# Performance work log

Hardware: AMD Instinct MI355X
Metric: run time of the kernel (lower is better)

Reference implementation:

```python
import jax, jax.numpy as jnp
import numpy as np

ITERS = 10


def setup_inputs() -> dict:
    key = jax.random.key(0)
    k0, k1 = jax.random.split(key)
    B, D, H, W = 4, 64, 64, 64
    feat0 = jax.random.normal(k0, (B, D, H, W), dtype=jnp.float32)
    feat1 = jax.random.normal(k1, (B, D, H, W), dtype=jnp.float32)
    bin_score = jnp.asarray(1.0, dtype=jnp.float32)  # learned scalar parameter
    return {"feat0": feat0, "feat1": feat1, "bin_score": bin_score}


def _cdist(x, y):
    # torch.cdist(p=2): euclidean distance between rows. x: [b,m,d], y: [b,n,d]
    x2 = jnp.sum(x * x, axis=-1)[:, :, None]          # [b,m,1]
    y2 = jnp.sum(y * y, axis=-1)[:, None, :]          # [b,1,n]
    xy = jnp.einsum('bmd,bnd->bmn', x, y)             # [b,m,n]
    d2 = jnp.maximum(x2 + y2 - 2.0 * xy, 0.0)
    return jnp.sqrt(d2)


def _log_sinkhorn(Z, log_mu, log_nu, iters):
    # Z: [b, m+1, n+1]; log_mu: [b, m+1]; log_nu: [b, n+1]
    u0 = jnp.zeros_like(log_mu)
    v0 = jnp.zeros_like(log_nu)

    def body(i, uv):
        u, v = uv
        u = log_mu - jax.nn.logsumexp(Z + v[:, None, :], axis=2)
        v = log_nu - jax.nn.logsumexp(Z + u[:, :, None], axis=1)
        return (u, v)

    u, v = jax.lax.fori_loop(0, iters, body, (u0, v0))
    return Z + u[:, :, None] + v[:, None, :]


def _forward(feat0, feat1, bin_score):
    b, d, h, w = feat0.shape
    f0 = feat0.transpose(0, 2, 3, 1).reshape(b, h * w, d)
    f1 = feat1.transpose(0, 2, 3, 1).reshape(b, h * w, d)
    distance = _cdist(f0, f1)                         # [b, m, n]
    m, n = h * w, h * w
    dt = distance.dtype

    bins0 = jnp.broadcast_to(bin_score, (b, m, 1)).astype(dt)
    bins1 = jnp.broadcast_to(bin_score, (b, 1, n)).astype(dt)
    binsa = jnp.broadcast_to(bin_score, (b, 1, 1)).astype(dt)
    couplings = jnp.concatenate([
        jnp.concatenate([distance, bins0], axis=-1),
        jnp.concatenate([bins1, binsa], axis=-1),
    ], axis=1)                                        # [b, m+1, n+1]

    ms = jnp.asarray(m, dt)
    ns = jnp.asarray(n, dt)
    norm = -jnp.log(ms + ns)
    log_mu = jnp.concatenate([jnp.full((m,), norm, dtype=dt), (jnp.log(ns) + norm)[None]])
    log_nu = jnp.concatenate([jnp.full((n,), norm, dtype=dt), (jnp.log(ms) + norm)[None]])
    log_mu = jnp.broadcast_to(log_mu[None], (b, m + 1))
    log_nu = jnp.broadcast_to(log_nu[None], (b, n + 1))

    Z = _log_sinkhorn(couplings, log_mu, log_nu, ITERS)
    Z = Z - norm
    gamma = jnp.exp(Z)                                # [b, m+1, n+1]

    matching_loss = jnp.mean(jnp.sum(gamma[:, :-1, :-1] * distance, axis=2))
    dustbin_loss = jnp.mean(gamma[:, :, -1]) + jnp.mean(gamma[:, :-1, :])
    return matching_loss, dustbin_loss, gamma


def reference(feat0, feat1, bin_score):
    return _forward(feat0, feat1, bin_score)
```

## Files before the change

kernel.cpp:

```cpp
#include <hip/hip_runtime.h>
#include <math.h>

#define BB 4
#define DD 64
#define MM 4096
#define M1 4097
#define NORMC 9.0109133472792788f
#define CSH 11.0f
#define SCLX 1.0e12f
#define INVSCLX 1.0e-12f

typedef __attribute__((ext_vector_type(8))) short bf16x8;
typedef __attribute__((ext_vector_type(4))) float f32x4;

__device__ __forceinline__ f32x4 mfma16(bf16x8 a, bf16x8 b, f32x4 c) {
    return __builtin_amdgcn_mfma_f32_16x16x32_bf16(a, b, c, 0, 0, 0);
}
__device__ __forceinline__ unsigned short f2bf(float x) {
    unsigned u = __float_as_uint(x);
    u += 0x7fffu + ((u >> 16) & 1u);
    return (unsigned short)(u >> 16);
}

__global__ void __launch_bounds__(256)
prep_kernel(const float* __restrict__ f0, const float* __restrict__ f1,
            unsigned short* __restrict__ h0, unsigned short* __restrict__ h1) {
    __shared__ float T[64][65];
    const int b = blockIdx.y;
    const int p0 = blockIdx.x * 64;
    const float* src = (blockIdx.z == 0 ? f0 : f1) + (size_t)b * DD * MM;
    unsigned short* dh = (blockIdx.z == 0 ? h0 : h1) + (size_t)b * MM * DD;
    const int tid = threadIdx.x;
#pragma unroll
    for (int l = 0; l < 16; ++l) {
        int idx = l * 256 + tid;
        T[idx >> 6][idx & 63] = src[(idx >> 6) * MM + p0 + (idx & 63)];
    }
    __syncthreads();
    const int p = tid >> 2;
    const int cs = (tid & 3) * 16;
    unsigned hw[8];
#pragma unroll
    for (int k = 0; k < 8; ++k) {
        unsigned short a = f2bf(T[cs + 2 * k][p]);
        unsigned short c = f2bf(T[cs + 2 * k + 1][p]);
        hw[k] = (unsigned)a | ((unsigned)c << 16);
    }
    size_t base = (size_t)(p0 + p) * DD + cs;
    *(uint4*)(dh + base)     = make_uint4(hw[0], hw[1], hw[2], hw[3]);
    *(uint4*)(dh + base + 8) = make_uint4(hw[4], hw[5], hw[6], hw[7]);
}

__global__ void __launch_bounds__(256)
norms_kernel(const float* __restrict__ f0, const float* __restrict__ f1,
             float* __restrict__ n0, float* __restrict__ n1,
             float* __restrict__ W, float* __restrict__ S) {
    int t = blockIdx.x * 256 + threadIdx.x;
    if (t >= BB * MM) return;
    int b = t / MM, p = t % MM;
    const float* s0 = f0 + (size_t)b * DD * MM + p;
    const float* s1 = f1 + (size_t)b * DD * MM + p;
    float a = 0.f, c = 0.f;
#pragma unroll 8
    for (int k = 0; k < DD; ++k) {
        float x = s0[(size_t)k * MM]; a = fmaf(x, x, a);
        float y = s1[(size_t)k * MM]; c = fmaf(y, y, c);
    }
    n0[t] = a; n1[t] = c;
    W[t] = 1.0f;
    if (t < 8) S[t] = 1.0f;
}

__global__ void __launch_bounds__(256)
distEB_kernel(const unsigned short* __restrict__ h0, const unsigned short* __restrict__ h1,
              const float* __restrict__ n0, const float* __restrict__ n1,
              uint2* __restrict__ EB) {
    __shared__ unsigned char sc[4][640];
    const int id = blockIdx.x;
    const int xcd = id & 7, slot = id >> 3;
    const int b = xcd >> 1;
    const int x = slot * 2 + (xcd & 1);
    const int r0 = x * 32;
    const int tid = threadIdx.x;
    const int w = tid >> 6, l = tid & 63, lg = l >> 4, lc = l & 15;
    const size_t fb = (size_t)b * MM * DD;

    bf16x8 Ah[2][2];
    float n0r[2][4];
#pragma unroll
    for (int st = 0; st < 2; ++st) {
        const unsigned short* pa = h0 + fb + (size_t)(r0 + st * 16 + lc) * DD + 8 * lg;
        Ah[st][0] = *(const bf16x8*)pa; Ah[st][1] = *(const bf16x8*)(pa + 32);
#pragma unroll
        for (int e = 0; e < 4; ++e)
            n0r[st][e] = n0[b * MM + r0 + st * 16 + 4 * lg + e];
    }

    for (int tt = 0; tt < 64; ++tt) {
        const int jt = w * 64 + tt;
        const int j0 = jt * 16;
        const unsigned short* pb = h1 + fb + (size_t)(j0 + lc) * DD + 8 * lg;
        bf16x8 Bh0 = *(const bf16x8*)pb, Bh1 = *(const bf16x8*)(pb + 32);
        float n1j = n1[b * MM + j0 + lc];
        unsigned pk[2];
#pragma unroll
        for (int st = 0; st < 2; ++st) {
            f32x4 acc = {0.f, 0.f, 0.f, 0.f};
            acc = mfma16(Ah[st][0], Bh0, acc);
            acc = mfma16(Ah[st][1], Bh1, acc);
            float Ev[4];
#pragma unroll
            for (int e = 0; e < 4; ++e) {
                float d2 = fmaxf(__builtin_fmaf(-2.f, acc[e], n0r[st][e] + n1j), 0.f);
                Ev[e] = __expf(sqrtf(d2) - CSH);
            }
            int p = __builtin_amdgcn_cvt_pk_fp8_f32(Ev[0], Ev[1], 0, false);
            p = __builtin_amdgcn_cvt_pk_fp8_f32(Ev[2], Ev[3], p, true);
            pk[st] = (unsigned)p;
        }
        *(unsigned*)&sc[w][lc * 40 + 4 * lg]      = pk[0];
        *(unsigned*)&sc[w][lc * 40 + 16 + 4 * lg] = pk[1];
        uint2 v = *(const uint2*)&sc[w][lc * 40 + 8 * lg];
        EB[(((size_t)(b * 128 + x)) * 256 + jt) * 64 + l] = v;
    }
}

__global__ void __launch_bounds__(512)
sinkEB_kernel(const uint2* __restrict__ EB, const float* __restrict__ W,
              float* __restrict__ X, float* __restrict__ S,
              float* __restrict__ psum, const float* __restrict__ bin) {
    const int bid = blockIdx.x;
    const int tid = threadIdx.x;
    const float bs = *bin;
    if (bid < BB) {
        __shared__ float am[8];
        const int b = bid;
        const int w = tid >> 6, l = tid & 63;
        float s = 0.f;
        for (int t = tid; t < MM; t += 512) s += W[b * MM + t];
#pragma unroll
        for (int off = 1; off < 64; off <<= 1) s += __shfl_xor(s, off);
        if (l == 0) am[w] = s;
        __syncthreads();
        if (tid == 0) {
            float tot = 0.f;
#pragma unroll
            for (int k = 0; k < 8; ++k) tot += am[k];
            S[b] = 0.5f * __expf(-bs) / (tot + S[4 + b]);
        }
        return;
    }
    __shared__ float Wl[4096];
    __shared__ float ps[256];
    __shared__ float XL[32];
    const int idx = bid - BB;
    const int b = idx >> 7, x = idx & 127;
    const int w = tid >> 6, l = tid & 63, lg = l >> 4, lc = l & 15;
    const float KC = __expf(-NORMC - CSH);
    const float wmm = __expf(bs - CSH) * S[4 + b];
#pragma unroll
    for (int k = 0; k < 8; ++k) Wl[k * 512 + tid] = W[b * MM + k * 512 + tid];
    __syncthreads();

    const uint2* EP = EB + (((size_t)(b * 128 + x)) * 256 + w * 32) * 64 + l;
    uint2 ec[32];
#pragma unroll
    for (int k = 0; k < 32; ++k) ec[k] = EP[(size_t)k * 64];

    float rs[8] = {};
#pragma unroll
    for (int k = 0; k < 32; ++k) {
        float wv = Wl[(w * 32 + k) * 16 + lc];
        auto p0 = __builtin_amdgcn_cvt_pk_f32_fp8((int)ec[k].x, false);
        auto p1 = __builtin_amdgcn_cvt_pk_f32_fp8((int)ec[k].x, true);
        auto p2 = __builtin_amdgcn_cvt_pk_f32_fp8((int)ec[k].y, false);
        auto p3 = __builtin_amdgcn_cvt_pk_f32_fp8((int)ec[k].y, true);
        rs[0] = fmaf(p0[0], wv, rs[0]); rs[1] = fmaf(p0[1], wv, rs[1]);
        rs[2] = fmaf(p1[0], wv, rs[2]); rs[3] = fmaf(p1[1], wv, rs[3]);
        rs[4] = fmaf(p2[0], wv, rs[4]); rs[5] = fmaf(p2[1], wv, rs[5]);
        rs[6] = fmaf(p3[0], wv, rs[6]); rs[7] = fmaf(p3[1], wv, rs[7]);
    }
#pragma unroll
    for (int off = 1; off < 16; off <<= 1)
#pragma unroll
        for (int t = 0; t < 8; ++t) rs[t] += __shfl_xor(rs[t], off);
    if (lc == 0) {
#pragma unroll
        for (int t = 0; t < 8; ++t) ps[w * 32 + 8 * lg + t] = rs[t];
    }
    __syncthreads();
    if (tid < 32) {
        float s = 0.f;
#pragma unroll
        for (int k = 0; k < 8; ++k) s += ps[k * 32 + tid];
        float xv = KC / (s + wmm);
        X[b * MM + x * 32 + tid] = xv;
        XL[tid] = xv * SCLX;
    }
    __syncthreads();

    float f0 = XL[8 * lg + 0], f1 = XL[8 * lg + 1];
    float f2 = XL[8 * lg + 2], f3 = XL[8 * lg + 3];
    float f4 = XL[8 * lg + 4], f5 = XL[8 * lg + 5];
    float f6 = XL[8 * lg + 6], f7 = XL[8 * lg + 7];
    int u0 = __builtin_amdgcn_cvt_pk_fp8_f32(f0, f1, 0, false);
    u0 = __builtin_amdgcn_cvt_pk_fp8_f32(f2, f3, u0, true);
    int u1 = __builtin_amdgcn_cvt_pk_fp8_f32(f4, f5, 0, false);
    u1 = __builtin_amdgcn_cvt_pk_fp8_f32(f6, f7, u1, true);
    long long av = (long long)(((unsigned long long)(unsigned)u1 << 32) | (unsigned)u0);
    float* po = psum + ((size_t)(b * 128 + x)) * MM;
    const f32x4 zero = {0.f, 0.f, 0.f, 0.f};
#pragma unroll
    for (int k = 0; k < 32; ++k) {
        long long bv = (long long)(((unsigned long long)ec[k].y << 32) | ec[k].x);
        f32x4 c = __builtin_amdgcn_mfma_f32_16x16x32_fp8_fp8(av, bv, zero, 0, 0, 0);
        if (l < 16) po[(w * 32 + k) * 16 + l] = c[0];
    }
}

__global__ void __launch_bounds__(256)
wcomb_kernel(const float* __restrict__ psum, const float* __restrict__ X,
             float* __restrict__ W, float* __restrict__ S,
             const float* __restrict__ bin) {
    const int bid = blockIdx.x;
    const int tid = threadIdx.x;
    const float bs = *bin;
    if (bid < BB * 64) {
        __shared__ float ps[256];
        const int b = bid >> 6, cg = bid & 63;
        const int c64 = tid & 63, g = tid >> 6;
        const float* pp = psum + ((size_t)(b * 128 + g * 32)) * MM + cg * 64 + c64;
        float s = 0.f;
#pragma unroll
        for (int c = 0; c < 32; ++c) s += pp[(size_t)c * MM];
        ps[tid] = s;
        __syncthreads();
        if (tid < 64) {
            float t = ps[tid] + ps[tid + 64] + ps[tid + 128] + ps[tid + 192];
            t = t * INVSCLX + __expf(bs - CSH) * S[b];
            W[b * MM + cg * 64 + tid] = __expf(-NORMC - CSH) / t;
        }
    } else {
        const int b = bid - BB * 64;
        const int w = tid >> 6, l = tid & 63;
        __shared__ float am[4];
        float s = 0.f;
        for (int t = tid; t < MM; t += 256) s += X[b * MM + t];
#pragma unroll
        for (int off = 1; off < 64; off <<= 1) s += __shfl_xor(s, off);
        if (l == 0) am[w] = s;
        __syncthreads();
        if (tid == 0) {
            float tot = am[0] + am[1] + am[2] + am[3];
            S[4 + b] = 0.5f * __expf(-bs) / (tot + S[b]);
        }
    }
}

__global__ void __launch_bounds__(256)
finEB_kernel(const uint2* __restrict__ EB, const float* __restrict__ X,
             const float* __restrict__ W, const float* __restrict__ S,
             const float* __restrict__ bin, float* __restrict__ G,
             float* __restrict__ pA, float* __restrict__ pB) {
    const int bid = blockIdx.x;
    const int tid = threadIdx.x;
    if (bid >= BB * 128) {
        const int eb = bid - BB * 128;
        const float bs = *bin;
        const float CC = __expf(NORMC + bs);
        int t = eb * 256 + tid;
        float pc = 0.f, pr = 0.f;
        if (t < BB * M1) {
            int b = t / M1, j = t % M1;
            float wj = (j < MM) ? W[b * MM + j] : S[4 + b];
            float g = CC * S[b] * wj;
            G[((size_t)b * M1 + MM) * M1 + j] = g;
            if (j == MM) pc += g;
        } else if (t < BB * M1 + BB * MM) {
            int q = t - BB * M1;
            int b = q / MM, i = q % MM;
            float g = CC * X[b * MM + i] * S[4 + b];
            G[((size_t)b * M1 + i) * M1 + MM] = g;
            pc += g; pr += g;
        }
#pragma unroll
        for (int off = 1; off < 64; off <<= 1) {
            pc += __shfl_xor(pc, off);
            pr += __shfl_xor(pr, off);
        }
        __shared__ float e0[4], e1[4];
        if ((tid & 63) == 0) { e0[tid >> 6] = pc; e1[tid >> 6] = pr; }
        __syncthreads();
        if (tid == 0) {
            pB[eb * 2 + 0] = e0[0] + e0[1] + e0[2] + e0[3];
            pB[eb * 2 + 1] = e1[0] + e1[1] + e1[2] + e1[3];
        }
        return;
    }
    __shared__ float T[256][36];
    __shared__ float Wl[4096];
    __shared__ float XL[32];
    const int b = bid >> 7, x = bid & 127;
    const int w = tid >> 6, l = tid & 63, lg = l >> 4, lc = l & 15;
#pragma unroll
    for (int k = 0; k < 16; ++k) Wl[k * 256 + tid] = W[b * MM + k * 256 + tid];
    if (tid < 32) XL[tid] = X[b * MM + x * 32 + tid] * __expf(NORMC + CSH);
    __syncthreads();

    const uint2* EBb = EB + ((size_t)(b * 128 + x)) * 256 * 64;
    float pm = 0.f, pr = 0.f;
    for (int ch = 0; ch < 16; ++ch) {
#pragma unroll
        for (int q = 0; q < 4; ++q) {
            const int jt = ch * 16 + w * 4 + q;
            uint2 ev = EBb[(size_t)jt * 64 + l];
            float wv = Wl[jt * 16 + lc];
            auto p0 = __builtin_amdgcn_cvt_pk_f32_fp8((int)ev.x, false);
            auto p1 = __builtin_amdgcn_cvt_pk_f32_fp8((int)ev.x, true);
            auto p2 = __builtin_amdgcn_cvt_pk_f32_fp8((int)ev.y, false);
            auto p3 = __builtin_amdgcn_cvt_pk_f32_fp8((int)ev.y, true);
            float Ef[8] = {p0[0], p0[1], p1[0], p1[1], p2[0], p2[1], p3[0], p3[1]};
            float g[8];
#pragma unroll
            for (int t = 0; t < 8; ++t) {
                g[t] = Ef[t] * XL[8 * lg + t] * wv;
                pm = fmaf(g[t], (Ef[t] > 0.f) ? (CSH + __logf(Ef[t])) : 0.f, pm);
                pr += g[t];
            }
            const int jl = (w * 4 + q) * 16 + lc;
            f32x4 v0 = {g[0], g[1], g[2], g[3]};
            f32x4 v1 = {g[4], g[5], g[6], g[7]};
            *(f32x4*)&T[jl][8 * lg]     = v0;
            *(f32x4*)&T[jl][8 * lg + 4] = v1;
        }
        __syncthreads();
        float* gb = G + ((size_t)(b * M1 + x * 32)) * M1 + ch * 256 + tid;
#pragma unroll
        for (int r = 0; r < 32; ++r) gb[(size_t)r * M1] = T[tid][r];
        __syncthreads();
    }
#pragma unroll
    for (int off = 1; off < 64; off <<= 1) {
        pm += __shfl_xor(pm, off);
        pr += __shfl_xor(pr, off);
    }
    __shared__ float s0[4], s1[4];
    if (l == 0) { s0[w] = pm; s1[w] = pr; }
    __syncthreads();
    if (tid == 0) {
        pA[bid * 2 + 0] = s0[0] + s0[1] + s0[2] + s0[3];
        pA[bid * 2 + 1] = s1[0] + s1[1] + s1[2] + s1[3];
    }
}

__global__ void __launch_bounds__(256)
reduce_out_kernel(const float* __restrict__ pA, int nA,
                  const float* __restrict__ pB, int nB, float* __restrict__ out) {
    const int tid = threadIdx.x;
    float pm = 0.f, prA = 0.f, pc = 0.f, prB = 0.f;
    for (int r = tid; r < nA; r += 256) { pm += pA[2 * r]; prA += pA[2 * r + 1]; }
    for (int r = tid; r < nB; r += 256) { pc += pB[2 * r]; prB += pB[2 * r + 1]; }
#pragma unroll
    for (int off = 1; off < 64; off <<= 1) {
        pm += __shfl_xor(pm, off);
        prA += __shfl_xor(prA, off);
        pc += __shfl_xor(pc, off);
        prB += __shfl_xor(prB, off);
    }
    __shared__ float a0[4], a1[4], a2[4], a3[4];
    if ((tid & 63) == 0) {
        int w = tid >> 6;
        a0[w] = pm; a1[w] = prA; a2[w] = pc; a3[w] = prB;
    }
    __syncthreads();
    if (tid == 0) {
        float PM = a0[0] + a0[1] + a0[2] + a0[3];
        float PRA = a1[0] + a1[1] + a1[2] + a1[3];
        float PC = a2[0] + a2[1] + a2[2] + a2[3];
        float PRB = a3[0] + a3[1] + a3[2] + a3[3];
        out[0] = PM / (4.0f * 4096.0f);
        out[1] = PC / (4.0f * 4097.0f) + (PRA + PRB) / (4.0f * 4096.0f * 4097.0f);
    }
}

extern "C" void kernel_launch(void* const* d_in, const int* in_sizes, int n_in,
                              void* d_out, int out_size, void* d_ws, size_t ws_size,
                              hipStream_t stream) {
    const float* feat0 = (const float*)d_in[0];
    const float* feat1 = (const float*)d_in[1];
    const float* bin   = (const float*)d_in[2];
    float* out = (float*)d_out;
    float* G   = out + 2;
    float* ws  = (float*)d_ws;

    const size_t OF_X   = 0;
    const size_t OF_W   = 16384;
    const size_t OF_S   = 32768;
    const size_t OF_PA  = 32832;
    const size_t OF_PB  = 33856;
    const size_t OF_N0  = 34128;
    const size_t OF_N1  = 50512;
    const size_t OF_PS  = 66896;
    const size_t OF_BF  = 2164048;
    const size_t OF_E8  = 3212624;

    float* X    = ws + OF_X;
    float* W    = ws + OF_W;
    float* S    = ws + OF_S;
    float* pA   = ws + OF_PA;
    float* pB   = ws + OF_PB;
    float* n0   = ws + OF_N0;
    float* n1   = ws + OF_N1;
    float* psum = ws + OF_PS;
    unsigned short* h0 = (unsigned short*)(ws + OF_BF);
    unsigned short* h1 = h0 + 1048576;
    uint2* EB = (uint2*)(ws + OF_E8);

    prep_kernel<<<dim3(64, BB, 2), 256, 0, stream>>>(feat0, feat1, h0, h1);
    norms_kernel<<<64, 256, 0, stream>>>(feat0, feat1, n0, n1, W, S);
    distEB_kernel<<<512, 256, 0, stream>>>(h0, h1, n0, n1, EB);
    for (int it = 0; it < 10; ++it) {
        sinkEB_kernel<<<BB + BB * 128, 512, 0, stream>>>(EB, W, X, S, psum, bin);
        wcomb_kernel<<<BB * 64 + BB, 256, 0, stream>>>(psum, X, W, S, bin);
    }
    finEB_kernel<<<BB * 128 + 129, 256, 0, stream>>>(EB, X, W, S, bin, G, pA, pB);
    reduce_out_kernel<<<1, 256, 0, stream>>>(pA, BB * 128, pB, 129, out);
}
```

Baseline: 384.0 us.

## Fuse Sinkhorn column combine into row kernel via atomic column sums

Removes the separate wcomb kernel per iteration by having each row block atomically add its column partial sums into a per-iteration buffer. The next iteration's kernel recomputes W and the dustbin scalars from those sums, which halves the launches per iteration and drops the large psum round trip through memory. The cost is that every block recomputes the full W vector and its reduction, and the atomics make the floating-point summation order nondeterministic. A memset now zeroes the per-iteration sum buffers.

```diff
diff --git a/kernel.cpp b/kernel.cpp
--- a/kernel.cpp
+++ b/kernel.cpp
@@ -53,8 +53,7 @@
 
 __global__ void __launch_bounds__(256)
 norms_kernel(const float* __restrict__ f0, const float* __restrict__ f1,
-             float* __restrict__ n0, float* __restrict__ n1,
-             float* __restrict__ W, float* __restrict__ S) {
+             float* __restrict__ n0, float* __restrict__ n1) {
     int t = blockIdx.x * 256 + threadIdx.x;
     if (t >= BB * MM) return;
     int b = t / MM, p = t % MM;
@@ -67,8 +66,6 @@
         float y = s1[(size_t)k * MM]; c = fmaf(y, y, c);
     }
     n0[t] = a; n1[t] = c;
-    W[t] = 1.0f;
-    if (t < 8) S[t] = 1.0f;
 }
 
 __global__ void __launch_bounds__(256)
@@ -126,41 +123,59 @@
 }
 
 __global__ void __launch_bounds__(512)
-sinkEB_kernel(const uint2* __restrict__ EB, const float* __restrict__ W,
-              float* __restrict__ X, float* __restrict__ S,
-              float* __restrict__ psum, const float* __restrict__ bin) {
-    const int bid = blockIdx.x;
-    const int tid = threadIdx.x;
-    const float bs = *bin;
-    if (bid < BB) {
-        __shared__ float am[8];
-        const int b = bid;
-        const int w = tid >> 6, l = tid & 63;
-        float s = 0.f;
-        for (int t = tid; t < MM; t += 512) s += W[b * MM + t];
-#pragma unroll
-        for (int off = 1; off < 64; off <<= 1) s += __shfl_xor(s, off);
-        if (l == 0) am[w] = s;
-        __syncthreads();
-        if (tid == 0) {
-            float tot = 0.f;
-#pragma unroll
-            for (int k = 0; k < 8; ++k) tot += am[k];
-            S[b] = 0.5f * __expf(-bs) / (tot + S[4 + b]);
-        }
-        return;
-    }
+sinkF_kernel(const uint2* __restrict__ EB,
+             const float* __restrict__ csPrev, float* __restrict__ csCur,
+             const float* __restrict__ sxpPrev, float* __restrict__ sxpCur,
+             const float* __restrict__ xmmPrev, float* __restrict__ xmmCur,
+             float* __restrict__ X, const float* __restrict__ bin, int first) {
     __shared__ float Wl[4096];
     __shared__ float ps[256];
     __shared__ float XL[32];
-    const int idx = bid - BB;
-    const int b = idx >> 7, x = idx & 127;
+    __shared__ float sh[8];
+    __shared__ float shWMM;
+    const int bid = blockIdx.x;
+    const int b = bid >> 7, x = bid & 127;
+    const int tid = threadIdx.x;
     const int w = tid >> 6, l = tid & 63, lg = l >> 4, lc = l & 15;
+    const float bs = *bin;
     const float KC = __expf(-NORMC - CSH);
-    const float wmm = __expf(bs - CSH) * S[4 + b];
-#pragma unroll
-    for (int k = 0; k < 8; ++k) Wl[k * 512 + tid] = W[b * MM + k * 512 + tid];
-    __syncthreads();
+    const float EBt = __expf(bs - CSH);
+    const float HB = 0.5f * __expf(-bs);
+
+    if (first) {
+#pragma unroll
+        for (int k = 0; k < 8; ++k) Wl[k * 512 + tid] = 1.0f;
+        if (tid == 0) shWMM = 1.0f;
+        if (l == 0) sh[w] = 512.f * 8.f / 8.f;
+    } else {
+        const float xmmP = xmmPrev[b];
+        if (tid < 64) {
+            float s = sxpPrev[b * 128 + tid] + sxpPrev[b * 128 + 64 + tid];
+#pragma unroll
+            for (int off = 1; off < 64; off <<= 1) s += __shfl_xor(s, off);
+            if (tid == 0) shWMM = HB / (s + xmmP);
+        }
+        const float db = EBt * xmmP;
+        float local = 0.f;
+#pragma unroll
+        for (int k = 0; k < 8; ++k) {
+            float cs = csPrev[b * MM + k * 512 + tid];
+            float wv = KC / fmaf(cs, INVSCLX, db);
+            Wl[k * 512 + tid] = wv;
+            local += wv;
+        }
+#pragma unroll
+        for (int off = 1; off < 64; off <<= 1) local += __shfl_xor(local, off);
+        if (l == 0) sh[w] = local;
+    }
+    __syncthreads();
+    const float wMMprev = shWMM;
+    const float wmmRow = EBt * wMMprev;
+    if (x == 0 && tid == 0) {
+        float sumW = ((sh[0] + sh[1]) + (sh[2] + sh[3]))
+                   + ((sh[4] + sh[5]) + (sh[6] + sh[7]));
+        xmmCur[b] = HB / (sumW + wMMprev);
+    }
 
     const uint2* EP = EB + (((size_t)(b * 128 + x)) * 256 + w * 32) * 64 + l;
     uint2 ec[32];
@@ -193,9 +208,13 @@
         float s = 0.f;
 #pragma unroll
         for (int k = 0; k < 8; ++k) s += ps[k * 32 + tid];
-        float xv = KC / (s + wmm);
+        float xv = KC / (s + wmmRow);
         X[b * MM + x * 32 + tid] = xv;
         XL[tid] = xv * SCLX;
+        float t = xv;
+#pragma unroll
+        for (int off = 1; off < 32; off <<= 1) t += __shfl_xor(t, off);
+        if (tid == 0) sxpCur[b * 128 + x] = t;
     }
     __syncthreads();
 
@@ -208,78 +227,51 @@
     int u1 = __builtin_amdgcn_cvt_pk_fp8_f32(f4, f5, 0, false);
     u1 = __builtin_amdgcn_cvt_pk_fp8_f32(f6, f7, u1, true);
     long long av = (long long)(((unsigned long long)(unsigned)u1 << 32) | (unsigned)u0);
-    float* po = psum + ((size_t)(b * 128 + x)) * MM;
     const f32x4 zero = {0.f, 0.f, 0.f, 0.f};
 #pragma unroll
     for (int k = 0; k < 32; ++k) {
         long long bv = (long long)(((unsigned long long)ec[k].y << 32) | ec[k].x);
         f32x4 c = __builtin_amdgcn_mfma_f32_16x16x32_fp8_fp8(av, bv, zero, 0, 0, 0);
-        if (l < 16) po[(w * 32 + k) * 16 + l] = c[0];
+        if (l < 16) atomicAdd(&csCur[b * MM + (w * 32 + k) * 16 + l], c[0]);
     }
 }
 
 __global__ void __launch_bounds__(256)
-wcomb_kernel(const float* __restrict__ psum, const float* __restrict__ X,
-             float* __restrict__ W, float* __restrict__ S,
-             const float* __restrict__ bin) {
+finF_kernel(const uint2* __restrict__ EB, const float* __restrict__ X,
+            const float* __restrict__ cs10, const float* __restrict__ sxp10,
+            const float* __restrict__ xmm10, const float* __restrict__ bin,
+            float* __restrict__ G, float* __restrict__ pA, float* __restrict__ pB) {
     const int bid = blockIdx.x;
     const int tid = threadIdx.x;
     const float bs = *bin;
-    if (bid < BB * 64) {
-        __shared__ float ps[256];
-        const int b = bid >> 6, cg = bid & 63;
-        const int c64 = tid & 63, g = tid >> 6;
-        const float* pp = psum + ((size_t)(b * 128 + g * 32)) * MM + cg * 64 + c64;
-        float s = 0.f;
-#pragma unroll
-        for (int c = 0; c < 32; ++c) s += pp[(size_t)c * MM];
-        ps[tid] = s;
+    const float KC = __expf(-NORMC - CSH);
+    const float EBt = __expf(bs - CSH);
+    const float HB = 0.5f * __expf(-bs);
+    if (bid >= BB * 128) {
+        __shared__ float wmm10s[4];
+        if (tid < 256) {
+            int bb = tid >> 6, ll = tid & 63;
+            float s = sxp10[bb * 128 + ll] + sxp10[bb * 128 + 64 + ll];
+#pragma unroll
+            for (int off = 1; off < 64; off <<= 1) s += __shfl_xor(s, off);
+            if (ll == 0) wmm10s[bb] = HB / (s + xmm10[bb]);
+        }
         __syncthreads();
-        if (tid < 64) {
-            float t = ps[tid] + ps[tid + 64] + ps[tid + 128] + ps[tid + 192];
-            t = t * INVSCLX + __expf(bs - CSH) * S[b];
-            W[b * MM + cg * 64 + tid] = __expf(-NORMC - CSH) / t;
-        }
-    } else {
-        const int b = bid - BB * 64;
-        const int w = tid >> 6, l = tid & 63;
-        __shared__ float am[4];
-        float s = 0.f;
-        for (int t = tid; t < MM; t += 256) s += X[b * MM + t];
-#pragma unroll
-        for (int off = 1; off < 64; off <<= 1) s += __shfl_xor(s, off);
-        if (l == 0) am[w] = s;
-        __syncthreads();
-        if (tid == 0) {
-            float tot = am[0] + am[1] + am[2] + am[3];
-            S[4 + b] = 0.5f * __expf(-bs) / (tot + S[b]);
-        }
-    }
-}
-
-__global__ void __launch_bounds__(256)
-finEB_kernel(const uint2* __restrict__ EB, const float* __restrict__ X,
-             const float* __restrict__ W, const float* __restrict__ S,
-             const float* __restrict__ bin, float* __restrict__ G,
-             float* __restrict__ pA, float* __restrict__ pB) {
-    const int bid = blockIdx.x;
-    const int tid = threadIdx.x;
-    if (bid >= BB * 128) {
         const int eb = bid - BB * 128;
-        const float bs = *bin;
         const float CC = __expf(NORMC + bs);
         int t = eb * 256 + tid;
         float pc = 0.f, pr = 0.f;
         if (t < BB * M1) {
             int b = t / M1, j = t % M1;
-            float wj = (j < MM) ? W[b * MM + j] : S[4 + b];
-            float g = CC * S[b] * wj;
+            float wj = (j < MM) ? KC / fmaf(cs10[b * MM + j], INVSCLX, EBt * xmm10[b])
+                                : wmm10s[b];
+            float g = CC * xmm10[b] * wj;
             G[((size_t)b * M1 + MM) * M1 + j] = g;
             if (j == MM) pc += g;
         } else if (t < BB * M1 + BB * MM) {
             int q = t - BB * M1;
             int b = q / MM, i = q % MM;
-            float g = CC * X[b * MM + i] * S[4 + b];
+            float g = CC * X[b * MM + i] * wmm10s[b];
             G[((size_t)b * M1 + i) * M1 + MM] = g;
             pc += g; pr += g;
         }
@@ -302,8 +294,14 @@
     __shared__ float XL[32];
     const int b = bid >> 7, x = bid & 127;
     const int w = tid >> 6, l = tid & 63, lg = l >> 4, lc = l & 15;
-#pragma unroll
-    for (int k = 0; k < 16; ++k) Wl[k * 256 + tid] = W[b * MM + k * 256 + tid];
+    {
+        const float db = EBt * xmm10[b];
+#pragma unroll
+        for (int k = 0; k < 16; ++k) {
+            float cs = cs10[b * MM + k * 256 + tid];
+            Wl[k * 256 + tid] = KC / fmaf(cs, INVSCLX, db);
+        }
+    }
     if (tid < 32) XL[tid] = X[b * MM + x * 32 + tid] * __expf(NORMC + CSH);
     __syncthreads();
 
@@ -394,35 +392,41 @@
     float* ws  = (float*)d_ws;
 
     const size_t OF_X   = 0;
-    const size_t OF_W   = 16384;
-    const size_t OF_S   = 32768;
-    const size_t OF_PA  = 32832;
-    const size_t OF_PB  = 33856;
-    const size_t OF_N0  = 34128;
-    const size_t OF_N1  = 50512;
-    const size_t OF_PS  = 66896;
-    const size_t OF_BF  = 2164048;
-    const size_t OF_E8  = 3212624;
-
-    float* X    = ws + OF_X;
-    float* W    = ws + OF_W;
-    float* S    = ws + OF_S;
-    float* pA   = ws + OF_PA;
-    float* pB   = ws + OF_PB;
-    float* n0   = ws + OF_N0;
-    float* n1   = ws + OF_N1;
-    float* psum = ws + OF_PS;
+    const size_t OF_XMM = 16384;
+    const size_t OF_SXP = 16448;
+    const size_t OF_CS  = 22080;
+    const size_t OF_PA  = 202304;
+    const size_t OF_PB  = 203328;
+    const size_t OF_N0  = 203616;
+    const size_t OF_N1  = 220000;
+    const size_t OF_BF  = 236384;
+    const size_t OF_E8  = 1284960;
+
+    float* X   = ws + OF_X;
+    float* XMM = ws + OF_XMM;
+    float* SXP = ws + OF_SXP;
+    float* CS  = ws + OF_CS;
+    float* pA  = ws + OF_PA;
+    float* pB  = ws + OF_PB;
+    float* n0  = ws + OF_N0;
+    float* n1  = ws + OF_N1;
     unsigned short* h0 = (unsigned short*)(ws + OF_BF);
     unsigned short* h1 = h0 + 1048576;
     uint2* EB = (uint2*)(ws + OF_E8);
 
+    hipMemsetAsync(CS, 0, 11 * 16384 * sizeof(float), stream);
     prep_kernel<<<dim3(64, BB, 2), 256, 0, stream>>>(feat0, feat1, h0, h1);
-    norms_kernel<<<64, 256, 0, stream>>>(feat0, feat1, n0, n1, W, S);
+    norms_kernel<<<64, 256, 0, stream>>>(feat0, feat1, n0, n1);
     distEB_kernel<<<512, 256, 0, stream>>>(h0, h1, n0, n1, EB);
-    for (int it = 0; it < 10; ++it) {
-        sinkEB_kernel<<<BB + BB * 128, 512, 0, stream>>>(EB, W, X, S, psum, bin);
-        wcomb_kernel<<<BB * 64 + BB, 256, 0, stream>>>(psum, X, W, S, bin);
-    }
-    finEB_kernel<<<BB * 128 + 129, 256, 0, stream>>>(EB, X, W, S, bin, G, pA, pB);
+    for (int k = 1; k <= 10; ++k) {
+        sinkF_kernel<<<512, 512, 0, stream>>>(
+            EB,
+            CS + (size_t)(k - 1) * 16384, CS + (size_t)k * 16384,
+            SXP + (size_t)(k - 1) * 512,  SXP + (size_t)k * 512,
+            XMM + (size_t)(k - 1) * 4,    XMM + (size_t)k * 4,
+            X, bin, (k == 1) ? 1 : 0);
+    }
+    finF_kernel<<<BB * 128 + 129, 256, 0, stream>>>(
+        EB, X, CS + 10 * 16384, SXP + 10 * 512, XMM + 10 * 4, bin, G, pA, pB);
     reduce_out_kernel<<<1, 256, 0, stream>>>(pA, BB * 128, pB, 129, out);
 }
```

New measurement: 395.1 us. 2.9% more time.
